# Kernel optimization log

Hardware: AMD Instinct MI355X
Metric: run time of the kernel (lower is better)

Reference implementation:

```python
import jax, jax.numpy as jnp
import numpy as np

B, Zc, Hin, Win = 256, 2048, 7, 7
S = 8            # SPATIAL_ : everything resized to 8x8
WIN = 2          # window_size
P = WIN * WIN    # 4 pixels per patch
N = (S // WIN) ** 2  # 16 patches
Q = 1            # ELM hidden neurons


def _lcg(m, n):
    """Deterministic LCG pseudo-random weights used by RADAM's RNN_AE."""
    L = m * n
    if L == 1:
        return np.ones((1, 1))
    V = np.zeros(L)
    V[0] = L + 1
    a, b, c = L + 2, L + 3, L * L
    for i in range(1, L):
        V[i] = (a * V[i - 1] + b) % c
    V = (V - V.mean()) / V.std()  # zscore (ddof=0, scipy default)
    return V.reshape(m, n)


def setup_inputs() -> dict:
    key = jax.random.key(0)
    x = jax.random.normal(key, (B, Zc, Hin, Win), dtype=jnp.float32)
    Wlcg = jnp.asarray(_lcg(Q, P + 1), dtype=jnp.float32)  # (Q, P+1) encoder weights incl. bias
    return {"x": x, "Wlcg": Wlcg}


def _zscore(a, axis):
    m = jnp.mean(a, axis=axis, keepdims=True)
    s = jnp.std(a, axis=axis, keepdims=True)  # ddof=0 like scipy.stats.zscore
    return jnp.nan_to_num((a - m) / s)


def reference(x, Wlcg):
    b, z = x.shape[:2]
    # torchvision Resize(8): bilinear resize to 8x8 (upsample here, antialias irrelevant)
    xr = jax.image.resize(x, (b, z, S, S), method="bilinear")
    # einops: 'b c (h p1) (w p2) -> b c (p1 p2) (h w)' with p1=p2=2
    g = S // WIN  # 4
    p = xr.reshape(b, z, g, WIN, g, WIN).transpose(0, 1, 3, 5, 2, 4).reshape(b, z, P, N)
    # stats.zscore over channel axis (axis=0 per sample) + nan_to_num
    p = _zscore(p, axis=1)
    # RNN_AE.fit: zscore each spectra over pixel axis (axis=0 of (P,N)) + nan_to_num
    Xc = _zscore(p, axis=2)                                   # (b, z, P, N)
    ones = jnp.ones((b, z, 1, N), Xc.dtype)
    Xb = jnp.concatenate([ones, Xc], axis=2)                  # (b, z, P+1, N) bias row
    hidden = jax.nn.sigmoid(jnp.einsum("qp,bzpn->bzqn", Wlcg, Xb))  # (b, z, Q, N)
    # closed-form AE decoder: beta = X Z^T (Z Z^T)^{-1}  (Q=1 -> scalar inverse)
    zz = jnp.sum(hidden * hidden, axis=-1, keepdims=True)     # (b, z, Q, 1)
    beta = jnp.einsum("bzpn,bzqn->bzpq", Xc, hidden) / jnp.swapaxes(zz, -1, -2)  # (b, z, P, Q)
    # std-pool decoder weights over pixel axis -> one scalar per channel
    feat = jnp.std(beta, axis=2)                              # (b, z, 1)
    return feat
```

## Files before the change

kernel.cpp:

```cpp
#include <hip/hip_runtime.h>
#include <math.h>

#define REC_LEN 49
#define RECS_PER_BLK 256
#define STAGE_FLOATS (RECS_PER_BLK * REC_LEN)
#define ZC 2048
#define NB 256
#define NPOS 64

__device__ __forceinline__ void patchvals(const float* __restrict__ in, float* __restrict__ out) {
    const float wA[8] = {1.f, 0.1875f, 0.3125f, 0.4375f, 0.5625f, 0.6875f, 0.8125f, 1.f};
    const float wB[8] = {0.f, 0.8125f, 0.6875f, 0.5625f, 0.4375f, 0.3125f, 0.1875f, 0.f};
    const int  i0[8]  = {0, 0, 1, 2, 3, 4, 5, 6};
    const int  i1[8]  = {0, 1, 2, 3, 4, 5, 6, 6};
#pragma unroll
    for (int r = 0; r < 8; ++r) {
        float tmp[7];
#pragma unroll
        for (int c = 0; c < 7; ++c)
            tmp[c] = wA[r] * in[i0[r] * 7 + c] + wB[r] * in[i1[r] * 7 + c];
#pragma unroll
        for (int c = 0; c < 8; ++c) {
            float v = wA[c] * tmp[i0[c]] + wB[c] * tmp[i1[c]];
            int k = (((r & 1) * 2 + (c & 1)) << 4) + ((r >> 1) << 2) + (c >> 1);
            out[k] = v;
        }
    }
}

extern "C" __global__ void __launch_bounds__(256)
k_stats(const float* __restrict__ x, float* __restrict__ part) {
    __shared__ float smem[16384];
    const int tid = threadIdx.x;

    const float4* s4 = (const float4*)(x + (size_t)blockIdx.x * STAGE_FLOATS);
    float4* l4 = (float4*)smem;
    for (int i = tid; i < STAGE_FLOATS / 4; i += 256) l4[i] = s4[i];
    __syncthreads();

    float in[REC_LEN];
#pragma unroll
    for (int j = 0; j < REC_LEN; ++j) in[j] = smem[tid * REC_LEN + j];
    __syncthreads();

    float v[NPOS];
    patchvals(in, v);

    const int sw = tid & 31;
#pragma unroll
    for (int k = 0; k < NPOS; ++k)
        smem[tid * NPOS + (k ^ sw)] = v[k];
    __syncthreads();

    const int k = tid & 63;
    const int g = tid >> 6;
    float S = 0.f, S2 = 0.f;
#pragma unroll 16
    for (int zi = g * 64; zi < g * 64 + 64; ++zi) {
        float t = smem[zi * NPOS + (k ^ (zi & 31))];
        S += t; S2 += t * t;
    }
    __syncthreads();
    smem[g * NPOS + (k ^ (g & 31))]            = S;
    smem[(4 + g) * NPOS + (k ^ ((4 + g) & 31))] = S2;
    __syncthreads();
    if (tid < 64) {
        float s = 0.f, s2 = 0.f;
#pragma unroll
        for (int g2 = 0; g2 < 4; ++g2) {
            s  += smem[g2 * NPOS + (tid ^ (g2 & 31))];
            s2 += smem[(4 + g2) * NPOS + (tid ^ ((4 + g2) & 31))];
        }
        part[((size_t)blockIdx.x * 2 + 0) * 64 + tid] = s;
        part[((size_t)blockIdx.x * 2 + 1) * 64 + tid] = s2;
    }
}

extern "C" __global__ void __launch_bounds__(256)
k_final(const float* __restrict__ x, const float* __restrict__ Wl,
        const float* __restrict__ part, float* __restrict__ out) {
    __shared__ float stg[STAGE_FLOATS];
    __shared__ float msh[NPOS], ish[NPOS];
    const int tid = threadIdx.x;
    const int b = blockIdx.x >> 3;

    const float4* s4 = (const float4*)(x + (size_t)blockIdx.x * STAGE_FLOATS);
    float4* l4 = (float4*)stg;
    for (int i = tid; i < STAGE_FLOATS / 4; i += 256) l4[i] = s4[i];

    if (tid < 64) {
        float s = 0.f, s2 = 0.f;
#pragma unroll
        for (int c = 0; c < 8; ++c) {
            const float* p = part + ((size_t)(b * 8 + c) * 2) * 64;
            s  += p[tid];
            s2 += p[64 + tid];
        }
        float m   = s * (1.f / 2048.f);
        float var = fmaf(-m, m, s2 * (1.f / 2048.f));
        msh[tid] = m;
        ish[tid] = var > 0.f ? rsqrtf(var) : 0.f;
    }
    __syncthreads();

    float in[REC_LEN];
#pragma unroll
    for (int j = 0; j < REC_LEN; ++j) in[j] = stg[tid * REC_LEN + j];

    float v[NPOS];
    patchvals(in, v);

#pragma unroll
    for (int k = 0; k < NPOS; ++k)
        v[k] = (v[k] - msh[k]) * ish[k];

    const float w0 = Wl[0], w1 = Wl[1], w2 = Wl[2], w3 = Wl[3], w4 = Wl[4];
    float zz = 0.f, sp0 = 0.f, sp1 = 0.f, sp2 = 0.f, sp3 = 0.f;
#pragma unroll
    for (int n = 0; n < 16; ++n) {
        float a0 = v[n], a1 = v[16 + n], a2 = v[32 + n], a3 = v[48 + n];
        float m4 = 0.25f * (a0 + a1 + a2 + a3);
        float d0 = a0 - m4, d1 = a1 - m4, d2 = a2 - m4, d3 = a3 - m4;
        float var4 = 0.25f * (d0 * d0 + d1 * d1 + d2 * d2 + d3 * d3);
        float inv4 = var4 > 0.f ? rsqrtf(var4) : 0.f;
        float x0 = d0 * inv4, x1 = d1 * inv4, x2 = d2 * inv4, x3 = d3 * inv4;
        float t = w0 + w1 * x0 + w2 * x1 + w3 * x2 + w4 * x3;
        float h = 1.f / (1.f + expf(-t));
        zz += h * h;
        sp0 += x0 * h; sp1 += x1 * h; sp2 += x2 * h; sp3 += x3 * h;
    }
    float izz = 1.f / zz;
    float b0 = sp0 * izz, b1 = sp1 * izz, b2 = sp2 * izz, b3 = sp3 * izz;
    float mb = 0.25f * (b0 + b1 + b2 + b3);
    float e0 = b0 - mb, e1 = b1 - mb, e2 = b2 - mb, e3 = b3 - mb;
    out[(size_t)blockIdx.x * 256 + tid] = sqrtf(0.25f * (e0 * e0 + e1 * e1 + e2 * e2 + e3 * e3));
}

extern "C" void kernel_launch(void* const* d_in, const int* in_sizes, int n_in,
                              void* d_out, int out_size, void* d_ws, size_t ws_size,
                              hipStream_t stream) {
    (void)in_sizes; (void)n_in; (void)out_size; (void)ws_size;
    const float* x  = (const float*)d_in[0];
    const float* Wl = (const float*)d_in[1];
    float* out  = (float*)d_out;
    float* part = (float*)d_ws;

    k_stats<<<2048, 256, 0, stream>>>(x, part);
    k_final<<<2048, 256, 0, stream>>>(x, Wl, part, out);
}
```

Baseline: 199.7 us.

## Load records directly from global memory and reduce stats with wave shuffles

Both kernels drop the large shared-memory staging buffer. Each thread now loads its 49-float record straight from global memory with aligned float4 reads, and the record-to-thread mapping is permuted to lane*4+wave so every float4 stays aligned. In k_stats, the per-channel sums and sums of squares are reduced across the 64 lanes with a butterfly shuffle fold instead of a transpose through shared memory. This removes shared-memory traffic and the 50KB+ LDS footprint that limited occupancy, at the cost of uncoalesced strided global loads, heavy register pressure and many shuffle instructions.

```diff
diff --git a/kernel.cpp b/kernel.cpp
--- a/kernel.cpp
+++ b/kernel.cpp
@@ -2,10 +2,6 @@
 #include <math.h>
 
 #define REC_LEN 49
-#define RECS_PER_BLK 256
-#define STAGE_FLOATS (RECS_PER_BLK * REC_LEN)
-#define ZC 2048
-#define NB 256
 #define NPOS 64
 
 __device__ __forceinline__ void patchvals(const float* __restrict__ in, float* __restrict__ out) {
@@ -21,78 +17,93 @@
             tmp[c] = wA[r] * in[i0[r] * 7 + c] + wB[r] * in[i1[r] * 7 + c];
 #pragma unroll
         for (int c = 0; c < 8; ++c) {
-            float v = wA[c] * tmp[i0[c]] + wB[c] * tmp[i1[c]];
+            float vv = wA[c] * tmp[i0[c]] + wB[c] * tmp[i1[c]];
             int k = (((r & 1) * 2 + (c & 1)) << 4) + ((r >> 1) << 2) + (c >> 1);
-            out[k] = v;
+            out[k] = vv;
+        }
+    }
+}
+
+template<int W>
+__device__ __forceinline__ void load_rec(const float* __restrict__ xblk, int lane, float* __restrict__ in) {
+    const float4* p = (const float4*)xblk + 49 * lane + 12 * W;
+    float4 f[13];
+#pragma unroll
+    for (int i = 0; i < 13; ++i) f[i] = p[i];
+    const float* ff = (const float*)f;
+#pragma unroll
+    for (int j = 0; j < 49; ++j) in[j] = ff[W + j];
+}
+
+#define LOAD_REC_SWITCH(xblk, lane, in, w)            \
+    switch (w) {                                      \
+        case 0:  load_rec<0>(xblk, lane, in); break;  \
+        case 1:  load_rec<1>(xblk, lane, in); break;  \
+        case 2:  load_rec<2>(xblk, lane, in); break;  \
+        default: load_rec<3>(xblk, lane, in); break;  \
+    }
+
+__device__ __forceinline__ void fold64(float* a, int lane) {
+#pragma unroll
+    for (int m = 32; m >= 1; m >>= 1) {
+        const bool hi = (lane & m) != 0;
+#pragma unroll
+        for (int i = 0; i < m; ++i) {
+            float x0 = a[i], x1 = a[i + m];
+            float mine  = hi ? x1 : x0;
+            float other = hi ? x0 : x1;
+            a[i] = mine + __shfl_xor(other, m, 64);
         }
     }
 }
 
 extern "C" __global__ void __launch_bounds__(256)
 k_stats(const float* __restrict__ x, float* __restrict__ part) {
-    __shared__ float smem[16384];
     const int tid = threadIdx.x;
-
-    const float4* s4 = (const float4*)(x + (size_t)blockIdx.x * STAGE_FLOATS);
-    float4* l4 = (float4*)smem;
-    for (int i = tid; i < STAGE_FLOATS / 4; i += 256) l4[i] = s4[i];
-    __syncthreads();
+    const int lane = tid & 63, w = tid >> 6;
+    const float* xblk = x + (size_t)blockIdx.x * (256 * REC_LEN);
 
     float in[REC_LEN];
-#pragma unroll
-    for (int j = 0; j < REC_LEN; ++j) in[j] = smem[tid * REC_LEN + j];
-    __syncthreads();
+    LOAD_REC_SWITCH(xblk, lane, in, w);
 
     float v[NPOS];
     patchvals(in, v);
+    float sq[NPOS];
+#pragma unroll
+    for (int k = 0; k < NPOS; ++k) sq[k] = v[k] * v[k];
 
-    const int sw = tid & 31;
-#pragma unroll
-    for (int k = 0; k < NPOS; ++k)
-        smem[tid * NPOS + (k ^ sw)] = v[k];
-    __syncthreads();
+    fold64(v, lane);
+    fold64(sq, lane);
 
-    const int k = tid & 63;
-    const int g = tid >> 6;
-    float S = 0.f, S2 = 0.f;
-#pragma unroll 16
-    for (int zi = g * 64; zi < g * 64 + 64; ++zi) {
-        float t = smem[zi * NPOS + (k ^ (zi & 31))];
-        S += t; S2 += t * t;
-    }
-    __syncthreads();
-    smem[g * NPOS + (k ^ (g & 31))]            = S;
-    smem[(4 + g) * NPOS + (k ^ ((4 + g) & 31))] = S2;
+    __shared__ float red[4][2][64];
+    red[w][0][lane] = v[0];
+    red[w][1][lane] = sq[0];
     __syncthreads();
     if (tid < 64) {
-        float s = 0.f, s2 = 0.f;
-#pragma unroll
-        for (int g2 = 0; g2 < 4; ++g2) {
-            s  += smem[g2 * NPOS + (tid ^ (g2 & 31))];
-            s2 += smem[(4 + g2) * NPOS + (tid ^ ((4 + g2) & 31))];
-        }
-        part[((size_t)blockIdx.x * 2 + 0) * 64 + tid] = s;
-        part[((size_t)blockIdx.x * 2 + 1) * 64 + tid] = s2;
+        float s  = red[0][0][tid] + red[1][0][tid] + red[2][0][tid] + red[3][0][tid];
+        float s2 = red[0][1][tid] + red[1][1][tid] + red[2][1][tid] + red[3][1][tid];
+        part[(size_t)blockIdx.x * 128 + tid]      = s;
+        part[(size_t)blockIdx.x * 128 + 64 + tid] = s2;
     }
 }
 
 extern "C" __global__ void __launch_bounds__(256)
 k_final(const float* __restrict__ x, const float* __restrict__ Wl,
         const float* __restrict__ part, float* __restrict__ out) {
-    __shared__ float stg[STAGE_FLOATS];
     __shared__ float msh[NPOS], ish[NPOS];
     const int tid = threadIdx.x;
+    const int lane = tid & 63, w = tid >> 6;
     const int b = blockIdx.x >> 3;
+    const float* xblk = x + (size_t)blockIdx.x * (256 * REC_LEN);
 
-    const float4* s4 = (const float4*)(x + (size_t)blockIdx.x * STAGE_FLOATS);
-    float4* l4 = (float4*)stg;
-    for (int i = tid; i < STAGE_FLOATS / 4; i += 256) l4[i] = s4[i];
+    float in[REC_LEN];
+    LOAD_REC_SWITCH(xblk, lane, in, w);
 
     if (tid < 64) {
         float s = 0.f, s2 = 0.f;
 #pragma unroll
         for (int c = 0; c < 8; ++c) {
-            const float* p = part + ((size_t)(b * 8 + c) * 2) * 64;
+            const float* p = part + (size_t)(b * 8 + c) * 128;
             s  += p[tid];
             s2 += p[64 + tid];
         }
@@ -102,10 +113,6 @@
         ish[tid] = var > 0.f ? rsqrtf(var) : 0.f;
     }
     __syncthreads();
-
-    float in[REC_LEN];
-#pragma unroll
-    for (int j = 0; j < REC_LEN; ++j) in[j] = stg[tid * REC_LEN + j];
 
     float v[NPOS];
     patchvals(in, v);
@@ -133,7 +140,8 @@
     float b0 = sp0 * izz, b1 = sp1 * izz, b2 = sp2 * izz, b3 = sp3 * izz;
     float mb = 0.25f * (b0 + b1 + b2 + b3);
     float e0 = b0 - mb, e1 = b1 - mb, e2 = b2 - mb, e3 = b3 - mb;
-    out[(size_t)blockIdx.x * 256 + tid] = sqrtf(0.25f * (e0 * e0 + e1 * e1 + e2 * e2 + e3 * e3));
+    out[(size_t)blockIdx.x * 256 + 4 * lane + w] =
+        sqrtf(0.25f * (e0 * e0 + e1 * e1 + e2 * e2 + e3 * e3));
 }
 
 extern "C" void kernel_launch(void* const* d_in, const int* in_sizes, int n_in,
```

Result: slower. 217.3 us (+8.8%).
